# Kernel optimization log

Measured on AMD Instinct MI355X. Metric: run time of the kernel, lower is better.

The kernel has to match this reference:

```python
import jax, jax.numpy as jnp
import numpy as np

B, S, D = 4, 1024, 1024
H, DK, DV = 16, 64, 64


def setup_inputs() -> dict:
    key = jax.random.key(0)
    ks = jax.random.split(key, 12)
    s = 0.02
    inp = {
        "Q": jax.random.normal(ks[0], (B, S, D), jnp.float32),
        "K": jax.random.normal(ks[1], (B, S, D), jnp.float32),
        "V": jax.random.normal(ks[2], (B, S, D), jnp.float32),
        "attn_mask": jnp.zeros((B, S, S), dtype=bool),
        "Wq": jax.random.normal(ks[3], (D, H * DK), jnp.float32) * s,
        "bq": jnp.zeros((H * DK,), jnp.float32),
        "Wk": jax.random.normal(ks[4], (D, H * DK), jnp.float32) * s,
        "bk": jnp.zeros((H * DK,), jnp.float32),
        "Wv": jax.random.normal(ks[5], (D, H * DV), jnp.float32) * s,
        "bv": jnp.zeros((H * DV,), jnp.float32),
        "Wout": jax.random.normal(ks[6], (H * DV, D), jnp.float32) * s,
        "bout": jnp.zeros((D,), jnp.float32),
        "ln_g": jnp.ones((D,), jnp.float32),
        "ln_b": jnp.zeros((D,), jnp.float32),
    }
    return inp


def _layernorm(x, g, b, eps=1e-5):
    mu = jnp.mean(x, axis=-1, keepdims=True)
    var = jnp.mean(jnp.square(x - mu), axis=-1, keepdims=True)
    return (x - mu) * jax.lax.rsqrt(var + eps) * g + b


def reference(Q, K, V, attn_mask, Wq, bq, Wk, bk, Wv, bv, Wout, bout, ln_g, ln_b):
    residual = Q
    # project and split heads: [B, H, S, d]
    q = (Q @ Wq + bq).reshape(B, S, H, DK).transpose(0, 2, 1, 3)
    k = (K @ Wk + bk).reshape(B, S, H, DK).transpose(0, 2, 1, 3)
    v = (V @ Wv + bv).reshape(B, S, H, DV).transpose(0, 2, 1, 3)
    scores = jnp.einsum("bhqd,bhkd->bhqk", q, k) / np.sqrt(DK).astype(np.float32)
    scores = jnp.where(attn_mask[:, None, :, :], jnp.float32(-1e9), scores)
    attn = jax.nn.softmax(scores, axis=-1)
    ctx = jnp.einsum("bhqk,bhkd->bhqd", attn, v)
    ctx = ctx.transpose(0, 2, 1, 3).reshape(B, S, H * DV)
    out = ctx @ Wout + bout
    out = _layernorm(out + residual, ln_g, ln_b)
    return out, attn
```

## Files before the change

kernel.cpp:

```cpp
#include <hip/hip_runtime.h>
#include <stdint.h>

typedef unsigned short u16;
typedef __bf16 bf8v __attribute__((ext_vector_type(8)));
typedef float f4v __attribute__((ext_vector_type(4)));

__device__ __forceinline__ u16 f2bf(float f) {
  uint32_t x = __float_as_uint(f);
  return (u16)((x + 0x7FFFu + ((x >> 16) & 1u)) >> 16);
}

#define GLDS16(gp, lp)                                                        \
  __builtin_amdgcn_global_load_lds(                                           \
      (const __attribute__((address_space(1))) void*)(const void*)(gp),       \
      (__attribute__((address_space(3))) void*)(void*)(lp), 16, 0, 0)

__global__ __launch_bounds__(256) void k_cvt_act(const float* __restrict__ Q,
                                                 const float* __restrict__ K,
                                                 const float* __restrict__ V,
                                                 u16* __restrict__ Qb,
                                                 u16* __restrict__ Kb,
                                                 u16* __restrict__ Vb) {
  const float* src = blockIdx.z == 0 ? Q : (blockIdx.z == 1 ? K : V);
  u16* dst = blockIdx.z == 0 ? Qb : (blockIdx.z == 1 ? Kb : Vb);
  size_t i = ((size_t)blockIdx.x * 256 + threadIdx.x) * 4;
  float4 v = *(const float4*)(src + i);
  ushort4 o;
  o.x = f2bf(v.x); o.y = f2bf(v.y); o.z = f2bf(v.z); o.w = f2bf(v.w);
  *(ushort4*)(dst + i) = o;
}

__global__ __launch_bounds__(256) void k_cvt_w(const float* __restrict__ W0, const float* __restrict__ W1,
                                               const float* __restrict__ W2, const float* __restrict__ W3,
                                               u16* __restrict__ T0, u16* __restrict__ T1,
                                               u16* __restrict__ T2, u16* __restrict__ T3) {
  int z = blockIdx.z;
  const float* W = z == 0 ? W0 : z == 1 ? W1 : z == 2 ? W2 : W3;
  u16* T = z == 0 ? T0 : z == 1 ? T1 : z == 2 ? T2 : T3;
  __shared__ float tile[64][65];
  int n0 = blockIdx.x * 64, k0 = blockIdx.y * 64;
  int t = threadIdx.x;
#pragma unroll
  for (int i = 0; i < 16; ++i) {
    int idx = i * 256 + t;
    int rk = idx >> 6, cn = idx & 63;
    tile[rk][cn] = W[(size_t)(k0 + rk) * 1024 + n0 + cn];
  }
  __syncthreads();
#pragma unroll
  for (int i = 0; i < 16; ++i) {
    int idx = i * 256 + t;
    int rn = idx >> 6, ck = idx & 63;
    T[(size_t)(n0 + rn) * 1024 + k0 + ck] = f2bf(tile[ck][rn]);
  }
}

__global__ __launch_bounds__(256) void k_proj(const u16* __restrict__ Qb, const u16* __restrict__ Kb,
                                              const u16* __restrict__ Vb,
                                              const u16* __restrict__ WqT, const u16* __restrict__ WkT,
                                              const u16* __restrict__ WvT,
                                              const float* __restrict__ bq, const float* __restrict__ bk,
                                              const float* __restrict__ bv,
                                              u16* __restrict__ qh, u16* __restrict__ kh,
                                              u16* __restrict__ vT) {
  int z = blockIdx.z;
  const u16* A = z == 0 ? Qb : z == 1 ? Kb : Vb;
  const u16* Bt = z == 0 ? WqT : z == 1 ? WkT : WvT;
  const float* bias = z == 0 ? bq : z == 1 ? bk : bv;
  u16* out = z == 0 ? qh : z == 1 ? kh : vT;
  bool vtrans = (z == 2);

  __shared__ __align__(16) u16 sA[128 * 64];
  __shared__ __align__(16) u16 sB[128 * 64];

  int m0 = blockIdx.y * 128, n0 = blockIdx.x * 128;
  int t = threadIdx.x, w = t >> 6, lane = t & 63;
  int col = lane & 15, quad = lane >> 4;

  f4v zero4 = {0.f, 0.f, 0.f, 0.f};
  f4v acc[2][8];
#pragma unroll
  for (int tm = 0; tm < 2; ++tm)
#pragma unroll
    for (int tn = 0; tn < 8; ++tn) acc[tm][tn] = zero4;

  for (int kt = 0; kt < 1024; kt += 64) {
#pragma unroll
    for (int i = 0; i < 4; ++i) {
      int seg = i * 4 + w;
      int e = seg * 512 + lane * 8;
      int r = e >> 6, c = e & 63;
      GLDS16(A + (size_t)(m0 + r) * 1024 + kt + c, sA + seg * 512);
      GLDS16(Bt + (size_t)(n0 + r) * 1024 + kt + c, sB + seg * 512);
    }
    __syncthreads();
#pragma unroll
    for (int ks = 0; ks < 2; ++ks) {
      bf8v af[2], bfr[8];
#pragma unroll
      for (int tm = 0; tm < 2; ++tm)
        af[tm] = *(const bf8v*)&sA[(w * 32 + tm * 16 + col) * 64 + ks * 32 + quad * 8];
#pragma unroll
      for (int tn = 0; tn < 8; ++tn)
        bfr[tn] = *(const bf8v*)&sB[(tn * 16 + col) * 64 + ks * 32 + quad * 8];
#pragma unroll
      for (int tm = 0; tm < 2; ++tm)
#pragma unroll
        for (int tn = 0; tn < 8; ++tn)
          acc[tm][tn] = __builtin_amdgcn_mfma_f32_16x16x32_bf16(af[tm], bfr[tn], acc[tm][tn], 0, 0, 0);
    }
    __syncthreads();
  }

#pragma unroll
  for (int tm = 0; tm < 2; ++tm)
#pragma unroll
    for (int tn = 0; tn < 8; ++tn)
#pragma unroll
      for (int r = 0; r < 4; ++r) {
        int gr = m0 + w * 32 + tm * 16 + quad * 4 + r;
        int gc = n0 + tn * 16 + col;
        float v = acc[tm][tn][r] + bias[gc];
        int b = gr >> 10, s = gr & 1023;
        int h = gc >> 6, d = gc & 63;
        size_t off = vtrans ? ((size_t)((b * 16 + h) * 64 + d) * 1024 + s)
                            : ((size_t)((b * 16 + h) * 1024 + s) * 64 + d);
        out[off] = f2bf(v);
      }
}

__global__ __launch_bounds__(256) void k_attnA(const u16* __restrict__ qh, const u16* __restrict__ kh,
                                               const unsigned char* __restrict__ mask,
                                               float* __restrict__ attn,
                                               float* __restrict__ statM, float* __restrict__ statL) {
  int qt = blockIdx.x, bh = blockIdx.y;
  int b = bh >> 4;
  __shared__ __align__(16) u16 sQ[128 * 64];
  __shared__ __align__(16) u16 sK[128 * 64];
  __shared__ __align__(16) unsigned char sM[128 * 128];
  int t = threadIdx.x, w = t >> 6, lane = t & 63;
  int col = lane & 15, quad = lane >> 4;

  {
    const u16* qbase = qh + ((size_t)bh * 1024 + qt * 128) * 64;
#pragma unroll
    for (int i = 0; i < 4; ++i) {
      int seg = i * 4 + w;
      GLDS16(qbase + seg * 512 + lane * 8, sQ + seg * 512);
    }
  }

  float mrun[2][4], lrun[2][4];
#pragma unroll
  for (int tm = 0; tm < 2; ++tm)
#pragma unroll
    for (int r = 0; r < 4; ++r) { mrun[tm][r] = -3.0e38f; lrun[tm][r] = 0.f; }

  f4v zero4 = {0.f, 0.f, 0.f, 0.f};

  for (int nc = 0; nc < 8; ++nc) {
    const u16* kbase = kh + ((size_t)bh * 1024 + nc * 128) * 64;
#pragma unroll
    for (int i = 0; i < 4; ++i) {
      int seg = i * 4 + w;
      GLDS16(kbase + seg * 512 + lane * 8, sK + seg * 512);
    }
    const unsigned char* mbase = mask + (size_t)b * 1024 * 1024 + (size_t)(qt * 128) * 1024 + nc * 128;
#pragma unroll
    for (int i = 0; i < 4; ++i) {
      int seg = i * 4 + w;
      int e = seg * 1024 + lane * 16;
      int r = e >> 7, c = e & 127;
      GLDS16(mbase + (size_t)r * 1024 + c, sM + seg * 1024);
    }
    __syncthreads();

    f4v acc[2][8];
#pragma unroll
    for (int tm = 0; tm < 2; ++tm)
#pragma unroll
      for (int tn = 0; tn < 8; ++tn) acc[tm][tn] = zero4;

#pragma unroll
    for (int ks = 0; ks < 2; ++ks) {
      bf8v af[2], bfr[8];
#pragma unroll
      for (int tm = 0; tm < 2; ++tm)
        af[tm] = *(const bf8v*)&sQ[(w * 32 + tm * 16 + col) * 64 + ks * 32 + quad * 8];
#pragma unroll
      for (int tn = 0; tn < 8; ++tn)
        bfr[tn] = *(const bf8v*)&sK[(tn * 16 + col) * 64 + ks * 32 + quad * 8];
#pragma unroll
      for (int tm = 0; tm < 2; ++tm)
#pragma unroll
        for (int tn = 0; tn < 8; ++tn)
          acc[tm][tn] = __builtin_amdgcn_mfma_f32_16x16x32_bf16(af[tm], bfr[tn], acc[tm][tn], 0, 0, 0);
    }

#pragma unroll
    for (int tm = 0; tm < 2; ++tm)
#pragma unroll
      for (int r = 0; r < 4; ++r) {
        int lrow = w * 32 + tm * 16 + quad * 4 + r;
        float vals[8];
        float cmax = -3.0e38f;
#pragma unroll
        for (int tn = 0; tn < 8; ++tn) {
          float v = acc[tm][tn][r] * 0.125f;
          if (sM[lrow * 128 + tn * 16 + col]) v = -1e9f;
          vals[tn] = v;
          cmax = fmaxf(cmax, v);
        }
#pragma unroll
        for (int off = 1; off < 16; off <<= 1) cmax = fmaxf(cmax, __shfl_xor(cmax, off));
        float csum = 0.f;
#pragma unroll
        for (int tn = 0; tn < 8; ++tn) csum += __expf(vals[tn] - cmax);
#pragma unroll
        for (int off = 1; off < 16; off <<= 1) csum += __shfl_xor(csum, off);
        float mo = mrun[tm][r];
        float mn = fmaxf(mo, cmax);
        lrun[tm][r] = lrun[tm][r] * __expf(mo - mn) + csum * __expf(cmax - mn);
        mrun[tm][r] = mn;
        float* arow = attn + ((size_t)bh * 1024 + (size_t)qt * 128 + lrow) * 1024 + nc * 128;
#pragma unroll
        for (int tn = 0; tn < 8; ++tn) arow[tn * 16 + col] = vals[tn];
      }
    __syncthreads();
  }

  if (col == 0) {
#pragma unroll
    for (int tm = 0; tm < 2; ++tm)
#pragma unroll
      for (int r = 0; r < 4; ++r) {
        size_t idx = (size_t)bh * 1024 + qt * 128 + w * 32 + tm * 16 + quad * 4 + r;
        statM[idx] = mrun[tm][r];
        statL[idx] = lrun[tm][r];
      }
  }
}

__global__ __launch_bounds__(256) void k_attnB(const u16* __restrict__ vT,
                                               const float* __restrict__ statM,
                                               const float* __restrict__ statL,
                                               float* __restrict__ attn, u16* __restrict__ ctx) {
  int qt = blockIdx.x, bh = blockIdx.y, b = bh >> 4, h = bh & 15;
  __shared__ __align__(16) u16 sP[128 * 128];
  __shared__ __align__(16) u16 sV[64 * 128];
  int t = threadIdx.x, w = t >> 6, lane = t & 63;
  int col = lane & 15, quad = lane >> 4;

  float m_r[2][4], linv[2][4];
#pragma unroll
  for (int tm = 0; tm < 2; ++tm)
#pragma unroll
    for (int r = 0; r < 4; ++r) {
      size_t idx = (size_t)bh * 1024 + qt * 128 + w * 32 + tm * 16 + quad * 4 + r;
      m_r[tm][r] = statM[idx];
      linv[tm][r] = 1.0f / statL[idx];
    }

  f4v zero4 = {0.f, 0.f, 0.f, 0.f};
  f4v acc[2][4];
#pragma unroll
  for (int tm = 0; tm < 2; ++tm)
#pragma unroll
    for (int tn = 0; tn < 4; ++tn) acc[tm][tn] = zero4;

  for (int kc = 0; kc < 8; ++kc) {
    float pv[2][4][8];
#pragma unroll
    for (int tm = 0; tm < 2; ++tm)
#pragma unroll
      for (int r = 0; r < 4; ++r) {
        float* arow = attn + ((size_t)bh * 1024 + (size_t)qt * 128 + w * 32 + tm * 16 + quad * 4 + r) * 1024 + kc * 128;
#pragma unroll
        for (int tn = 0; tn < 8; ++tn) {
          float s = arow[tn * 16 + col];
          float p = __expf(s - m_r[tm][r]) * linv[tm][r];
          arow[tn * 16 + col] = p;
          pv[tm][r][tn] = p;
        }
      }
    __syncthreads();
    const u16* vbase = vT + (size_t)bh * 64 * 1024 + kc * 128;
#pragma unroll
    for (int i = 0; i < 4; ++i) {
      int seg = i * 4 + w;
      int e = seg * 512 + lane * 8;
      GLDS16(vbase + (size_t)(e >> 7) * 1024 + (e & 127), sV + seg * 512);
    }
#pragma unroll
    for (int tm = 0; tm < 2; ++tm)
#pragma unroll
      for (int r = 0; r < 4; ++r)
#pragma unroll
        for (int tn = 0; tn < 8; ++tn)
          sP[(w * 32 + tm * 16 + quad * 4 + r) * 128 + tn * 16 + col] = f2bf(pv[tm][r][tn]);
    __syncthreads();
#pragma unroll
    for (int ks = 0; ks < 4; ++ks) {
      bf8v af[2], bfr[4];
#pragma unroll
      for (int tm = 0; tm < 2; ++tm)
        af[tm] = *(const bf8v*)&sP[(w * 32 + tm * 16 + col) * 128 + ks * 32 + quad * 8];
#pragma unroll
      for (int tn = 0; tn < 4; ++tn)
        bfr[tn] = *(const bf8v*)&sV[(tn * 16 + col) * 128 + ks * 32 + quad * 8];
#pragma unroll
      for (int tm = 0; tm < 2; ++tm)
#pragma unroll
        for (int tn = 0; tn < 4; ++tn)
          acc[tm][tn] = __builtin_amdgcn_mfma_f32_16x16x32_bf16(af[tm], bfr[tn], acc[tm][tn], 0, 0, 0);
    }
  }

#pragma unroll
  for (int tm = 0; tm < 2; ++tm)
#pragma unroll
    for (int tn = 0; tn < 4; ++tn)
#pragma unroll
      for (int r = 0; r < 4; ++r) {
        int token = qt * 128 + w * 32 + tm * 16 + quad * 4 + r;
        ctx[(size_t)(b * 1024 + token) * 1024 + h * 64 + tn * 16 + col] = f2bf(acc[tm][tn][r]);
      }
}

__global__ __launch_bounds__(256) void k_outproj(const u16* __restrict__ ctx, const u16* __restrict__ WoT,
                                                 const float* __restrict__ bout,
                                                 const float* __restrict__ Qres, float* __restrict__ y) {
  __shared__ __align__(16) u16 sA[128 * 64];
  __shared__ __align__(16) u16 sB[128 * 64];
  int m0 = blockIdx.y * 128, n0 = blockIdx.x * 128;
  int t = threadIdx.x, w = t >> 6, lane = t & 63;
  int col = lane & 15, quad = lane >> 4;

  f4v zero4 = {0.f, 0.f, 0.f, 0.f};
  f4v acc[2][8];
#pragma unroll
  for (int tm = 0; tm < 2; ++tm)
#pragma unroll
    for (int tn = 0; tn < 8; ++tn) acc[tm][tn] = zero4;

  for (int kt = 0; kt < 1024; kt += 64) {
#pragma unroll
    for (int i = 0; i < 4; ++i) {
      int seg = i * 4 + w;
      int e = seg * 512 + lane * 8;
      int r = e >> 6, c = e & 63;
      GLDS16(ctx + (size_t)(m0 + r) * 1024 + kt + c, sA + seg * 512);
      GLDS16(WoT + (size_t)(n0 + r) * 1024 + kt + c, sB + seg * 512);
    }
    __syncthreads();
#pragma unroll
    for (int ks = 0; ks < 2; ++ks) {
      bf8v af[2], bfr[8];
#pragma unroll
      for (int tm = 0; tm < 2; ++tm)
        af[tm] = *(const bf8v*)&sA[(w * 32 + tm * 16 + col) * 64 + ks * 32 + quad * 8];
#pragma unroll
      for (int tn = 0; tn < 8; ++tn)
        bfr[tn] = *(const bf8v*)&sB[(tn * 16 + col) * 64 + ks * 32 + quad * 8];
#pragma unroll
      for (int tm = 0; tm < 2; ++tm)
#pragma unroll
        for (int tn = 0; tn < 8; ++tn)
          acc[tm][tn] = __builtin_amdgcn_mfma_f32_16x16x32_bf16(af[tm], bfr[tn], acc[tm][tn], 0, 0, 0);
    }
    __syncthreads();
  }

#pragma unroll
  for (int tm = 0; tm < 2; ++tm)
#pragma unroll
    for (int tn = 0; tn < 8; ++tn)
#pragma unroll
      for (int r = 0; r < 4; ++r) {
        int gr = m0 + w * 32 + tm * 16 + quad * 4 + r;
        int gc = n0 + tn * 16 + col;
        float v = acc[tm][tn][r] + bout[gc] + Qres[(size_t)gr * 1024 + gc];
        y[(size_t)gr * 1024 + gc] = v;
      }
}

__global__ __launch_bounds__(256) void k_ln(const float* __restrict__ y, const float* __restrict__ g,
                                            const float* __restrict__ bb, float* __restrict__ out) {
  int r = blockIdx.x, t = threadIdx.x;
  const float* row = y + (size_t)r * 1024;
  float4 v = ((const float4*)row)[t];
  float s = v.x + v.y + v.z + v.w;
  float sq = v.x * v.x + v.y * v.y + v.z * v.z + v.w * v.w;
#pragma unroll
  for (int off = 1; off < 64; off <<= 1) {
    s += __shfl_xor(s, off);
    sq += __shfl_xor(sq, off);
  }
  __shared__ float ss[4], ssq[4];
  if ((t & 63) == 0) { ss[t >> 6] = s; ssq[t >> 6] = sq; }
  __syncthreads();
  s = ss[0] + ss[1] + ss[2] + ss[3];
  sq = ssq[0] + ssq[1] + ssq[2] + ssq[3];
  float mu = s * (1.f / 1024.f);
  float var = sq * (1.f / 1024.f) - mu * mu;
  float rst = rsqrtf(var + 1e-5f);
  float4 gg = ((const float4*)g)[t];
  float4 bv = ((const float4*)bb)[t];
  float4 o;
  o.x = (v.x - mu) * rst * gg.x + bv.x;
  o.y = (v.y - mu) * rst * gg.y + bv.y;
  o.z = (v.z - mu) * rst * gg.z + bv.z;
  o.w = (v.w - mu) * rst * gg.w + bv.w;
  ((float4*)(out + (size_t)r * 1024))[t] = o;
}

extern "C" void kernel_launch(void* const* d_in, const int* in_sizes, int n_in,
                              void* d_out, int out_size, void* d_ws, size_t ws_size,
                              hipStream_t stream) {
  (void)in_sizes; (void)n_in; (void)out_size; (void)ws_size;
  const float* Q = (const float*)d_in[0];
  const float* K = (const float*)d_in[1];
  const float* V = (const float*)d_in[2];
  const unsigned char* mask = (const unsigned char*)d_in[3];
  const float* Wq = (const float*)d_in[4];
  const float* bq = (const float*)d_in[5];
  const float* Wk = (const float*)d_in[6];
  const float* bk = (const float*)d_in[7];
  const float* Wv = (const float*)d_in[8];
  const float* bv = (const float*)d_in[9];
  const float* Wout = (const float*)d_in[10];
  const float* bout = (const float*)d_in[11];
  const float* lng = (const float*)d_in[12];
  const float* lnb = (const float*)d_in[13];

  u16* Qb = (u16*)d_ws;
  u16* Kb = Qb + 4194304;
  u16* Vb = Kb + 4194304;
  u16* WqT = Vb + 4194304;
  u16* WkT = WqT + 1048576;
  u16* WvT = WkT + 1048576;
  u16* WoT = WvT + 1048576;
  u16* qh = WoT + 1048576;
  u16* kh = qh + 4194304;
  u16* vT = kh + 4194304;
  u16* ctx = vT + 4194304;
  float* statM = (float*)(ctx + 4194304);
  float* statL = statM + 65536;
  float* y = statL + 65536;

  float* outp = (float*)d_out;
  float* attn = outp + 4194304;

  k_cvt_act<<<dim3(4096, 1, 3), 256, 0, stream>>>(Q, K, V, Qb, Kb, Vb);
  k_cvt_w<<<dim3(16, 16, 4), 256, 0, stream>>>(Wq, Wk, Wv, Wout, WqT, WkT, WvT, WoT);
  k_proj<<<dim3(8, 32, 3), 256, 0, stream>>>(Qb, Kb, Vb, WqT, WkT, WvT, bq, bk, bv, qh, kh, vT);
  k_attnA<<<dim3(8, 64), 256, 0, stream>>>(qh, kh, mask, attn, statM, statL);
  k_attnB<<<dim3(8, 64), 256, 0, stream>>>(vT, statM, statL, attn, ctx);
  k_outproj<<<dim3(8, 32), 256, 0, stream>>>(ctx, WoT, bout, Q, y);
  k_ln<<<dim3(4096), 256, 0, stream>>>(y, lng, lnb, outp);
}
```

Measured before the change: 620.9 us.

## Recompute QK^T in second attention pass instead of round-tripping scores through HBM

The first attention pass now only computes the row max and sum statistics and no longer stores raw scores to the attention output. The second pass reloads Q, K and the mask, recomputes the masked scaled scores with MFMA, normalizes them, and writes the final probabilities once before the PV product. This removes one full write and one full read of the large fp32 attention matrix, at the cost of a second QK^T matmul, a second mask read, and extra shared memory in the second pass.

Result: faster. 556.4 us (-10.4%).

```diff
diff --git a/kernel.cpp b/kernel.cpp
--- a/kernel.cpp
+++ b/kernel.cpp
@@ -131,7 +131,6 @@
 
 __global__ __launch_bounds__(256) void k_attnA(const u16* __restrict__ qh, const u16* __restrict__ kh,
                                                const unsigned char* __restrict__ mask,
-                                               float* __restrict__ attn,
                                                float* __restrict__ statM, float* __restrict__ statL) {
   int qt = blockIdx.x, bh = blockIdx.y;
   int b = bh >> 4;
@@ -170,8 +169,7 @@
     for (int i = 0; i < 4; ++i) {
       int seg = i * 4 + w;
       int e = seg * 1024 + lane * 16;
-      int r = e >> 7, c = e & 127;
-      GLDS16(mbase + (size_t)r * 1024 + c, sM + seg * 1024);
+      GLDS16(mbase + (size_t)(e >> 7) * 1024 + (e & 127), sM + seg * 1024);
     }
     __syncthreads();
 
@@ -222,9 +220,6 @@
         float mn = fmaxf(mo, cmax);
         lrun[tm][r] = lrun[tm][r] * __expf(mo - mn) + csum * __expf(cmax - mn);
         mrun[tm][r] = mn;
-        float* arow = attn + ((size_t)bh * 1024 + (size_t)qt * 128 + lrow) * 1024 + nc * 128;
-#pragma unroll
-        for (int tn = 0; tn < 8; ++tn) arow[tn * 16 + col] = vals[tn];
       }
     __syncthreads();
   }
@@ -241,15 +236,28 @@
   }
 }
 
-__global__ __launch_bounds__(256) void k_attnB(const u16* __restrict__ vT,
+__global__ __launch_bounds__(256) void k_attnB(const u16* __restrict__ qh, const u16* __restrict__ kh,
+                                               const u16* __restrict__ vT,
+                                               const unsigned char* __restrict__ mask,
                                                const float* __restrict__ statM,
                                                const float* __restrict__ statL,
                                                float* __restrict__ attn, u16* __restrict__ ctx) {
   int qt = blockIdx.x, bh = blockIdx.y, b = bh >> 4, h = bh & 15;
+  __shared__ __align__(16) u16 sQ[128 * 64];
+  __shared__ __align__(16) u16 sKV[128 * 64];
   __shared__ __align__(16) u16 sP[128 * 128];
-  __shared__ __align__(16) u16 sV[64 * 128];
+  __shared__ __align__(16) unsigned char sM[128 * 128];
   int t = threadIdx.x, w = t >> 6, lane = t & 63;
   int col = lane & 15, quad = lane >> 4;
+
+  {
+    const u16* qbase = qh + ((size_t)bh * 1024 + qt * 128) * 64;
+#pragma unroll
+    for (int i = 0; i < 4; ++i) {
+      int seg = i * 4 + w;
+      GLDS16(qbase + seg * 512 + lane * 8, sQ + seg * 512);
+    }
+  }
 
   float m_r[2][4], linv[2][4];
 #pragma unroll
@@ -269,36 +277,83 @@
     for (int tn = 0; tn < 4; ++tn) acc[tm][tn] = zero4;
 
   for (int kc = 0; kc < 8; ++kc) {
-    float pv[2][4][8];
+    __syncthreads();
+    {
+      const u16* kbase = kh + ((size_t)bh * 1024 + kc * 128) * 64;
+#pragma unroll
+      for (int i = 0; i < 4; ++i) {
+        int seg = i * 4 + w;
+        GLDS16(kbase + seg * 512 + lane * 8, sKV + seg * 512);
+      }
+      const unsigned char* mbase = mask + (size_t)b * 1024 * 1024 + (size_t)(qt * 128) * 1024 + kc * 128;
+#pragma unroll
+      for (int i = 0; i < 4; ++i) {
+        int seg = i * 4 + w;
+        int e = seg * 1024 + lane * 16;
+        GLDS16(mbase + (size_t)(e >> 7) * 1024 + (e & 127), sM + seg * 1024);
+      }
+    }
+    __syncthreads();
+
+    float p[2][4][8];
+    {
+      f4v accs[2][8];
+#pragma unroll
+      for (int tm = 0; tm < 2; ++tm)
+#pragma unroll
+        for (int tn = 0; tn < 8; ++tn) accs[tm][tn] = zero4;
+#pragma unroll
+      for (int ks = 0; ks < 2; ++ks) {
+        bf8v af[2], bfr[8];
+#pragma unroll
+        for (int tm = 0; tm < 2; ++tm)
+          af[tm] = *(const bf8v*)&sQ[(w * 32 + tm * 16 + col) * 64 + ks * 32 + quad * 8];
+#pragma unroll
+        for (int tn = 0; tn < 8; ++tn)
+          bfr[tn] = *(const bf8v*)&sKV[(tn * 16 + col) * 64 + ks * 32 + quad * 8];
+#pragma unroll
+        for (int tm = 0; tm < 2; ++tm)
+#pragma unroll
+          for (int tn = 0; tn < 8; ++tn)
+            accs[tm][tn] = __builtin_amdgcn_mfma_f32_16x16x32_bf16(af[tm], bfr[tn], accs[tm][tn], 0, 0, 0);
+      }
+#pragma unroll
+      for (int tm = 0; tm < 2; ++tm)
+#pragma unroll
+        for (int r = 0; r < 4; ++r) {
+          int lrow = w * 32 + tm * 16 + quad * 4 + r;
+#pragma unroll
+          for (int tn = 0; tn < 8; ++tn) {
+            float v = accs[tm][tn][r] * 0.125f;
+            if (sM[lrow * 128 + tn * 16 + col]) v = -1e9f;
+            float pp = __expf(v - m_r[tm][r]) * linv[tm][r];
+            p[tm][r][tn] = pp;
+            sP[lrow * 128 + tn * 16 + col] = f2bf(pp);
+          }
+        }
+    }
+    __syncthreads();
+
+    {
+      const u16* vbase = vT + (size_t)bh * 64 * 1024 + kc * 128;
+#pragma unroll
+      for (int i = 0; i < 4; ++i) {
+        int seg = i * 4 + w;
+        int e = seg * 512 + lane * 8;
+        GLDS16(vbase + (size_t)(e >> 7) * 1024 + (e & 127), sKV + seg * 512);
+      }
+    }
+    __syncthreads();
+
 #pragma unroll
     for (int tm = 0; tm < 2; ++tm)
 #pragma unroll
       for (int r = 0; r < 4; ++r) {
         float* arow = attn + ((size_t)bh * 1024 + (size_t)qt * 128 + w * 32 + tm * 16 + quad * 4 + r) * 1024 + kc * 128;
 #pragma unroll
-        for (int tn = 0; tn < 8; ++tn) {
-          float s = arow[tn * 16 + col];
-          float p = __expf(s - m_r[tm][r]) * linv[tm][r];
-          arow[tn * 16 + col] = p;
-          pv[tm][r][tn] = p;
-        }
-      }
-    __syncthreads();
-    const u16* vbase = vT + (size_t)bh * 64 * 1024 + kc * 128;
-#pragma unroll
-    for (int i = 0; i < 4; ++i) {
-      int seg = i * 4 + w;
-      int e = seg * 512 + lane * 8;
-      GLDS16(vbase + (size_t)(e >> 7) * 1024 + (e & 127), sV + seg * 512);
-    }
-#pragma unroll
-    for (int tm = 0; tm < 2; ++tm)
-#pragma unroll
-      for (int r = 0; r < 4; ++r)
-#pragma unroll
-        for (int tn = 0; tn < 8; ++tn)
-          sP[(w * 32 + tm * 16 + quad * 4 + r) * 128 + tn * 16 + col] = f2bf(pv[tm][r][tn]);
-    __syncthreads();
+        for (int tn = 0; tn < 8; ++tn) arow[tn * 16 + col] = p[tm][r][tn];
+      }
+
 #pragma unroll
     for (int ks = 0; ks < 4; ++ks) {
       bf8v af[2], bfr[4];
@@ -307,7 +362,7 @@
         af[tm] = *(const bf8v*)&sP[(w * 32 + tm * 16 + col) * 128 + ks * 32 + quad * 8];
 #pragma unroll
       for (int tn = 0; tn < 4; ++tn)
-        bfr[tn] = *(const bf8v*)&sV[(tn * 16 + col) * 128 + ks * 32 + quad * 8];
+        bfr[tn] = *(const bf8v*)&sKV[(tn * 16 + col) * 128 + ks * 32 + quad * 8];
 #pragma unroll
       for (int tm = 0; tm < 2; ++tm)
 #pragma unroll
@@ -454,8 +509,8 @@
   k_cvt_act<<<dim3(4096, 1, 3), 256, 0, stream>>>(Q, K, V, Qb, Kb, Vb);
   k_cvt_w<<<dim3(16, 16, 4), 256, 0, stream>>>(Wq, Wk, Wv, Wout, WqT, WkT, WvT, WoT);
   k_proj<<<dim3(8, 32, 3), 256, 0, stream>>>(Qb, Kb, Vb, WqT, WkT, WvT, bq, bk, bv, qh, kh, vT);
-  k_attnA<<<dim3(8, 64), 256, 0, stream>>>(qh, kh, mask, attn, statM, statL);
-  k_attnB<<<dim3(8, 64), 256, 0, stream>>>(vT, statM, statL, attn, ctx);
+  k_attnA<<<dim3(8, 64), 256, 0, stream>>>(qh, kh, mask, statM, statL);
+  k_attnB<<<dim3(8, 64), 256, 0, stream>>>(qh, kh, vT, mask, statM, statL, attn, ctx);
   k_outproj<<<dim3(8, 32), 256, 0, stream>>>(ctx, WoT, bout, Q, y);
   k_ln<<<dim3(4096), 256, 0, stream>>>(y, lng, lnb, outp);
 }
```
